# Optimization experiments

Hardware: AMD Instinct MI355X
Metric: run time of the kernel (lower is better)

The kernel has to match this reference:

```python
import jax, jax.numpy as jnp
import numpy as np

B, C_IN, V, C_OUT, K = 4, 64, 50000, 128, 7


def setup_inputs() -> dict:
    key = jax.random.key(0)
    k1, k2, k3, k4 = jax.random.split(key, 4)
    x = jax.random.normal(k1, (B, C_IN, V, 1), dtype=jnp.float32)
    # Gi: per-vertex [self, n1, n2, n3] indices (random neighbors, in-range)
    Gi = jax.random.randint(k2, (B, V, 4), 0, V, dtype=jnp.int64)
    # Conv2d(in, out, kernel=(1,7)) weight collapsed to [out, in, 7]
    W = jax.random.normal(k3, (C_OUT, C_IN, K), dtype=jnp.float32) * 0.05
    b = jax.random.normal(k4, (C_OUT,), dtype=jnp.float32) * 0.05
    return {"x": x, "Gi": Gi, "W": W, "b": b}


def reference(x, Gi, W, b):
    xs = x[..., 0]  # [B, C, V]  (squeeze(-1))
    Bx, C, Vx = xs.shape
    # prepend zero-padding column (index 0 after Gi+1 maps padded -1 entries)
    xp = jnp.concatenate([jnp.zeros((Bx, C, 1), xs.dtype), xs], axis=2)  # [B,C,V+1]
    gi = Gi + 1
    # gather per batch: f[b,c,v,j] = xp[b,c,gi[b,v,j]]
    f = jax.vmap(lambda xb, gb: xb[:, gb])(xp, gi)  # [B, C, V, 4]
    f0, f1, f2, f3 = f[..., 0], f[..., 1], f[..., 2], f[..., 3]
    G = jnp.stack([
        f0,
        f1 + f2 + f3,                                        # symm_oper 1
        f1 * f2 * f3,                                        # symm_oper 2
        f1 * f2 + f1 * f3 + f2 * f3,                         # symm_oper 3
        f1 * f1 + f2 * f2 + f3 * f3,                         # symm_oper 4
        jnp.abs(f1 - f2) + jnp.abs(f1 - f3) + jnp.abs(f2 - f3),  # symm_oper 5
        f1 * f1 * f1 + f2 * f2 * f2 + f3 * f3 * f3,          # symm_oper 6
    ], axis=3)  # [B, C, V, 7]
    # conv2d with kernel (1,7), no padding -> width collapses to 1
    out = jnp.einsum('bcvk,ock->bov', G, W) + b[None, :, None]
    return out[..., None]  # [B, C_out, V, 1]
```

## Files before the change

kernel.cpp:

```cpp
#include <hip/hip_runtime.h>
#include <cstdint>
#include <cstddef>

#define BB   4
#define CIN  64
#define VV   50000
#define COUT 128
#define NV   32
#define KTOT 448
#define KT   14
#define PITCH 456

typedef __attribute__((ext_vector_type(8))) short    short8;
typedef __attribute__((ext_vector_type(8))) _Float16 half8;
typedef __attribute__((ext_vector_type(4))) _Float16 half4;
typedef __attribute__((ext_vector_type(4))) float    f32x4;

__device__ _Float16       g_xt[(size_t)BB * VV * CIN];
__device__ unsigned short g_wb[KT * 8 * 64 * 8];

__device__ inline unsigned short f2h(float f) {
    union { _Float16 h; unsigned short u; } cv;
    cv.h = (_Float16)f;
    return cv.u;
}

__global__ __launch_bounds__(256) void transpose_k(const float* __restrict__ x) {
    __shared__ float tile[64][65];
    int b  = blockIdx.y;
    int v0 = blockIdx.x * 64;
    int t  = threadIdx.x;
    int tv = t & 15;
    int tc = t >> 4;
#pragma unroll
    for (int i = 0; i < 4; i++) {
        int c = tc + 16 * i;
        int v = v0 + tv * 4;
        const float* src = x + ((size_t)b * CIN + c) * VV + v;
        float4 f;
        if (v + 3 < VV) {
            f = *(const float4*)src;
        } else {
            f.x = v + 0 < VV ? src[0] : 0.f;
            f.y = v + 1 < VV ? src[1] : 0.f;
            f.z = v + 2 < VV ? src[2] : 0.f;
            f.w = v + 3 < VV ? src[3] : 0.f;
        }
        tile[c][tv * 4 + 0] = f.x;
        tile[c][tv * 4 + 1] = f.y;
        tile[c][tv * 4 + 2] = f.z;
        tile[c][tv * 4 + 3] = f.w;
    }
    __syncthreads();
    int c8  = t & 7;
    int tvv = t >> 3;
#pragma unroll
    for (int i = 0; i < 2; i++) {
        int v = v0 + tvv + 32 * i;
        if (v < VV) {
            union { _Float16 h[8]; short8 s; } u;
#pragma unroll
            for (int j = 0; j < 8; j++)
                u.h[j] = (_Float16)tile[c8 * 8 + j][tvv + 32 * i];
            *(short8*)(g_xt + ((size_t)b * VV + v) * CIN + c8 * 8) = u.s;
        }
    }
}

__global__ __launch_bounds__(256) void pack_wb_k(const float* __restrict__ W) {
    int idx = blockIdx.x * 256 + threadIdx.x;
    if (idx >= KT * 8 * 64) return;
    int lane = idx & 63;
    int mt   = (idx >> 6) & 7;
    int kt   = idx >> 9;
    int m    = mt * 16 + (lane & 15);
    int kb   = kt * 32 + (lane >> 4) * 8;
    union { unsigned short s[8]; short8 v; } u;
#pragma unroll
    for (int j = 0; j < 8; j++) {
        int kk = kb + j;
        int c  = kk & 63;
        int k  = kk >> 6;
        u.s[j] = f2h(W[((size_t)m * CIN + c) * 7 + k]);
    }
    *(short8*)&g_wb[(size_t)idx * 8] = u.v;
}

__device__ inline void feats(float f0, float f1, float f2, float f3, float* g) {
    g[0] = f0;
    g[1] = f1 + f2 + f3;
    float p12 = f1 * f2, p13 = f1 * f3, p23 = f2 * f3;
    g[2] = p12 * f3;
    g[3] = p12 + p13 + p23;
    g[4] = f1 * f1 + f2 * f2 + f3 * f3;
    g[5] = fabsf(f1 - f2) + fabsf(f1 - f3) + fabsf(f2 - f3);
    g[6] = f1 * f1 * f1 + f2 * f2 * f2 + f3 * f3 * f3;
}

__global__ __launch_bounds__(256) void mesh_k(
        const void* __restrict__ Gi, const float* __restrict__ bias,
        float* __restrict__ out) {
    __shared__ _Float16 Gl[NV * PITCH];
    __shared__ int Sidx[NV][4];

    int b  = blockIdx.y;
    int v0 = blockIdx.x * NV;
    int t  = threadIdx.x;

    const unsigned* gu = (const unsigned*)Gi;
    bool is64 = ((gu[1] | gu[3] | gu[5] | gu[7]) == 0u);

    if (t < NV * 4) {
        int vv = t >> 2, j = t & 3;
        int v  = v0 + vv;
        long long val = 0;
        if (v < VV) {
            size_t gb = ((size_t)b * VV + v) * 4 + j;
            val = is64 ? ((const long long*)Gi)[gb] : (long long)((const int*)Gi)[gb];
        }
        Sidx[vv][j] = (int)(val < 0 ? 0 : (val >= VV ? VV - 1 : val));
    }
    __syncthreads();

    int c4   = t & 15;
    int slot = t >> 4;
    int J[2][4];
#pragma unroll
    for (int p = 0; p < 2; ++p) {
        int vv = slot + p * 16;
#pragma unroll
        for (int j = 0; j < 4; ++j) J[p][j] = Sidx[vv][j];
    }
    const _Float16* base = g_xt + (size_t)b * VV * CIN + c4 * 4;
    half4 F[2][4];
#pragma unroll
    for (int p = 0; p < 2; ++p)
#pragma unroll
        for (int j = 0; j < 4; ++j)
            F[p][j] = *(const half4*)(base + (size_t)J[p][j] * CIN);

#pragma unroll
    for (int p = 0; p < 2; ++p) {
        int vv = slot + p * 16;
        float gc[4][7];
#pragma unroll
        for (int i = 0; i < 4; ++i)
            feats((float)F[p][0][i], (float)F[p][1][i],
                  (float)F[p][2][i], (float)F[p][3][i], gc[i]);
        _Float16* grow = &Gl[vv * PITCH + c4 * 4];
#pragma unroll
        for (int k = 0; k < 7; k++) {
            union { _Float16 h[4]; half4 v; } u;
#pragma unroll
            for (int i = 0; i < 4; ++i) u.h[i] = (_Float16)gc[i][k];
            *(half4*)(grow + k * 64) = u.v;
        }
    }
    __syncthreads();

    int w    = t >> 6;
    int lane = t & 63;
    int l15  = lane & 15;
    int q    = lane >> 4;

    f32x4 acc[2][2] = {};

    const half8* wb = (const half8*)g_wb;
#pragma unroll 2
    for (int kt = 0; kt < KT; ++kt) {
        half8 a0 = wb[(kt * 8 + 2 * w    ) * 64 + lane];
        half8 a1 = wb[(kt * 8 + 2 * w + 1) * 64 + lane];
        half8 b0 = *(const half8*)&Gl[(l15     ) * PITCH + kt * 32 + q * 8];
        half8 b1 = *(const half8*)&Gl[(l15 + 16) * PITCH + kt * 32 + q * 8];
        acc[0][0] = __builtin_amdgcn_mfma_f32_16x16x32_f16(a0, b0, acc[0][0], 0, 0, 0);
        acc[0][1] = __builtin_amdgcn_mfma_f32_16x16x32_f16(a0, b1, acc[0][1], 0, 0, 0);
        acc[1][0] = __builtin_amdgcn_mfma_f32_16x16x32_f16(a1, b0, acc[1][0], 0, 0, 0);
        acc[1][1] = __builtin_amdgcn_mfma_f32_16x16x32_f16(a1, b1, acc[1][1], 0, 0, 0);
    }

#pragma unroll
    for (int mt = 0; mt < 2; ++mt) {
        int o = 32 * w + mt * 16 + q * 4;
        float bs[4];
#pragma unroll
        for (int r = 0; r < 4; ++r) bs[r] = bias[o + r];
#pragma unroll
        for (int nt = 0; nt < 2; ++nt) {
            int v = v0 + nt * 16 + l15;
            if (v < VV) {
                float* po = out + ((size_t)b * COUT + o) * VV + v;
#pragma unroll
                for (int r = 0; r < 4; ++r)
                    po[(size_t)r * VV] = acc[mt][nt][r] + bs[r];
            }
        }
    }
}

extern "C" void kernel_launch(void* const* d_in, const int* in_sizes, int n_in,
                              void* d_out, int out_size, void* d_ws, size_t ws_size,
                              hipStream_t stream) {
    const float* x    = (const float*)d_in[0];
    const void*  Gi   = d_in[1];
    const float* W    = (const float*)d_in[2];
    const float* bias = (const float*)d_in[3];
    float* out        = (float*)d_out;

    dim3 gt((VV + 63) / 64, BB);
    transpose_k<<<gt, 256, 0, stream>>>(x);
    pack_wb_k<<<(KT * 8 * 64 + 255) / 256, 256, 0, stream>>>(W);
    dim3 gm((VV + NV - 1) / NV, BB);
    mesh_k<<<gm, 256, 0, stream>>>(Gi, bias, out);
}
```

Measured before the change: 205.0 us.

## Fold weight packing into transpose kernel, widen gathers, use nontemporal loads/stores

Weight packing moves into the transpose kernel, which removes one kernel launch. The mesh kernel now gathers 8 fp16 channels per thread (half8) for a single vertex, replacing the 4-channel loads spread over two vertices, which halves the number of gather instructions. Nontemporal loads for x and Gi and nontemporal stores for the output are meant to cut cache pollution from streaming data. The trade-off is more register use per thread.

```diff
diff --git a/kernel.cpp b/kernel.cpp
--- a/kernel.cpp
+++ b/kernel.cpp
@@ -13,7 +13,6 @@
 
 typedef __attribute__((ext_vector_type(8))) short    short8;
 typedef __attribute__((ext_vector_type(8))) _Float16 half8;
-typedef __attribute__((ext_vector_type(4))) _Float16 half4;
 typedef __attribute__((ext_vector_type(4))) float    f32x4;
 
 __device__ _Float16       g_xt[(size_t)BB * VV * CIN];
@@ -25,7 +24,28 @@
     return cv.u;
 }
 
-__global__ __launch_bounds__(256) void transpose_k(const float* __restrict__ x) {
+__global__ __launch_bounds__(256) void transpose_k(const float* __restrict__ x,
+                                                   const float* __restrict__ W) {
+    if (blockIdx.y == 0 && blockIdx.x < (KT * 8 * 64 + 255) / 256) {
+        int idx = blockIdx.x * 256 + threadIdx.x;
+        if (idx < KT * 8 * 64) {
+            int lane = idx & 63;
+            int mt   = (idx >> 6) & 7;
+            int kt   = idx >> 9;
+            int m    = mt * 16 + (lane & 15);
+            int kb   = kt * 32 + (lane >> 4) * 8;
+            union { unsigned short s[8]; short8 v; } u;
+#pragma unroll
+            for (int j = 0; j < 8; j++) {
+                int kk = kb + j;
+                int c  = kk & 63;
+                int k  = kk >> 6;
+                u.s[j] = f2h(W[((size_t)m * CIN + c) * 7 + k]);
+            }
+            *(short8*)&g_wb[(size_t)idx * 8] = u.v;
+        }
+    }
+
     __shared__ float tile[64][65];
     int b  = blockIdx.y;
     int v0 = blockIdx.x * 64;
@@ -37,19 +57,19 @@
         int c = tc + 16 * i;
         int v = v0 + tv * 4;
         const float* src = x + ((size_t)b * CIN + c) * VV + v;
-        float4 f;
+        f32x4 f;
         if (v + 3 < VV) {
-            f = *(const float4*)src;
+            f = __builtin_nontemporal_load((const f32x4*)src);
         } else {
-            f.x = v + 0 < VV ? src[0] : 0.f;
-            f.y = v + 1 < VV ? src[1] : 0.f;
-            f.z = v + 2 < VV ? src[2] : 0.f;
-            f.w = v + 3 < VV ? src[3] : 0.f;
-        }
-        tile[c][tv * 4 + 0] = f.x;
-        tile[c][tv * 4 + 1] = f.y;
-        tile[c][tv * 4 + 2] = f.z;
-        tile[c][tv * 4 + 3] = f.w;
+            f[0] = v + 0 < VV ? src[0] : 0.f;
+            f[1] = v + 1 < VV ? src[1] : 0.f;
+            f[2] = v + 2 < VV ? src[2] : 0.f;
+            f[3] = v + 3 < VV ? src[3] : 0.f;
+        }
+        tile[c][tv * 4 + 0] = f[0];
+        tile[c][tv * 4 + 1] = f[1];
+        tile[c][tv * 4 + 2] = f[2];
+        tile[c][tv * 4 + 3] = f[3];
     }
     __syncthreads();
     int c8  = t & 7;
@@ -65,25 +85,6 @@
             *(short8*)(g_xt + ((size_t)b * VV + v) * CIN + c8 * 8) = u.s;
         }
     }
-}
-
-__global__ __launch_bounds__(256) void pack_wb_k(const float* __restrict__ W) {
-    int idx = blockIdx.x * 256 + threadIdx.x;
-    if (idx >= KT * 8 * 64) return;
-    int lane = idx & 63;
-    int mt   = (idx >> 6) & 7;
-    int kt   = idx >> 9;
-    int m    = mt * 16 + (lane & 15);
-    int kb   = kt * 32 + (lane >> 4) * 8;
-    union { unsigned short s[8]; short8 v; } u;
-#pragma unroll
-    for (int j = 0; j < 8; j++) {
-        int kk = kb + j;
-        int c  = kk & 63;
-        int k  = kk >> 6;
-        u.s[j] = f2h(W[((size_t)m * CIN + c) * 7 + k]);
-    }
-    *(short8*)&g_wb[(size_t)idx * 8] = u.v;
 }
 
 __device__ inline void feats(float f0, float f1, float f2, float f3, float* g) {
@@ -116,46 +117,37 @@
         long long val = 0;
         if (v < VV) {
             size_t gb = ((size_t)b * VV + v) * 4 + j;
-            val = is64 ? ((const long long*)Gi)[gb] : (long long)((const int*)Gi)[gb];
+            val = is64 ? __builtin_nontemporal_load((const long long*)Gi + gb)
+                       : (long long)__builtin_nontemporal_load((const int*)Gi + gb);
         }
         Sidx[vv][j] = (int)(val < 0 ? 0 : (val >= VV ? VV - 1 : val));
     }
     __syncthreads();
 
-    int c4   = t & 15;
-    int slot = t >> 4;
-    int J[2][4];
-#pragma unroll
-    for (int p = 0; p < 2; ++p) {
-        int vv = slot + p * 16;
-#pragma unroll
-        for (int j = 0; j < 4; ++j) J[p][j] = Sidx[vv][j];
-    }
-    const _Float16* base = g_xt + (size_t)b * VV * CIN + c4 * 4;
-    half4 F[2][4];
-#pragma unroll
-    for (int p = 0; p < 2; ++p)
-#pragma unroll
-        for (int j = 0; j < 4; ++j)
-            F[p][j] = *(const half4*)(base + (size_t)J[p][j] * CIN);
-
-#pragma unroll
-    for (int p = 0; p < 2; ++p) {
-        int vv = slot + p * 16;
-        float gc[4][7];
-#pragma unroll
-        for (int i = 0; i < 4; ++i)
-            feats((float)F[p][0][i], (float)F[p][1][i],
-                  (float)F[p][2][i], (float)F[p][3][i], gc[i]);
-        _Float16* grow = &Gl[vv * PITCH + c4 * 4];
-#pragma unroll
-        for (int k = 0; k < 7; k++) {
-            union { _Float16 h[4]; half4 v; } u;
-#pragma unroll
-            for (int i = 0; i < 4; ++i) u.h[i] = (_Float16)gc[i][k];
-            *(half4*)(grow + k * 64) = u.v;
-        }
-    }
+    int c8   = t & 7;
+    int slot = t >> 3;
+    int J[4];
+#pragma unroll
+    for (int j = 0; j < 4; ++j) J[j] = Sidx[slot][j];
+
+    const _Float16* base = g_xt + (size_t)b * VV * CIN + c8 * 8;
+    half8 F[4];
+#pragma unroll
+    for (int j = 0; j < 4; ++j)
+        F[j] = *(const half8*)(base + (size_t)J[j] * CIN);
+
+    union { _Float16 h[8]; short8 s; } u[7];
+#pragma unroll
+    for (int i = 0; i < 8; ++i) {
+        float g7[7];
+        feats((float)F[0][i], (float)F[1][i], (float)F[2][i], (float)F[3][i], g7);
+#pragma unroll
+        for (int k = 0; k < 7; ++k) u[k].h[i] = (_Float16)g7[k];
+    }
+    _Float16* grow = &Gl[slot * PITCH + c8 * 8];
+#pragma unroll
+    for (int k = 0; k < 7; ++k)
+        *(short8*)(grow + k * 64) = u[k].s;
     __syncthreads();
 
     int w    = t >> 6;
@@ -185,13 +177,13 @@
 #pragma unroll
         for (int r = 0; r < 4; ++r) bs[r] = bias[o + r];
 #pragma unroll
-        for (int nt = 0; nt < 2; ++nt) {
-            int v = v0 + nt * 16 + l15;
+        for (int n = 0; n < 2; ++n) {
+            int v = v0 + n * 16 + l15;
             if (v < VV) {
                 float* po = out + ((size_t)b * COUT + o) * VV + v;
 #pragma unroll
                 for (int r = 0; r < 4; ++r)
-                    po[(size_t)r * VV] = acc[mt][nt][r] + bs[r];
+                    __builtin_nontemporal_store(acc[mt][n][r] + bs[r], po + (size_t)r * VV);
             }
         }
     }
@@ -207,8 +199,7 @@
     float* out        = (float*)d_out;
 
     dim3 gt((VV + 63) / 64, BB);
-    transpose_k<<<gt, 256, 0, stream>>>(x);
-    pack_wb_k<<<(KT * 8 * 64 + 255) / 256, 256, 0, stream>>>(W);
+    transpose_k<<<gt, 256, 0, stream>>>(x, W);
     dim3 gm((VV + NV - 1) / NV, BB);
     mesh_k<<<gm, 256, 0, stream>>>(Gi, bias, out);
 }
```

Measured after the change: 197.5 us. -3.7%, faster.
